# Optimization experiments

Measured on AMD Instinct MI355X. Metric: run time of the kernel, lower is better.

## Reference

```python
import jax, jax.numpy as jnp
import numpy as np

N_E = 1024
E_DIM = 64
BETA = 0.25


def setup_inputs() -> dict:
    key = jax.random.key(0)
    k1, k2 = jax.random.split(key)
    z = jax.random.normal(k1, (32, E_DIM, 32, 32), dtype=jnp.float32)
    embedding = jax.random.uniform(k2, (N_E, E_DIM), dtype=jnp.float32,
                                   minval=-1.0 / N_E, maxval=1.0 / N_E)
    return {"z": z, "embedding": embedding}


def reference(z, embedding):
    beta = BETA
    bt, ch, h, w = z.shape
    n_e = embedding.shape[0]
    # BCHW -> BHWC, flatten to [N, e_dim]
    zp = jnp.transpose(z, (0, 2, 3, 1))
    zf = zp.reshape(-1, ch)
    # squared L2 distances to each codebook entry: [N, n_e]
    d = (jnp.sum(zf ** 2, axis=1, keepdims=True)
         + jnp.sum(embedding ** 2, axis=1)
         - 2.0 * jnp.matmul(zf, embedding.T))
    idx = jnp.argmin(d, axis=1)                      # [N]
    min_encodings = jax.nn.one_hot(idx, n_e, dtype=jnp.float32)  # [N, n_e]
    # gather codebook rows (equivalent to one_hot @ embedding)
    z_q = embedding[idx].reshape(zp.shape)           # [B,H,W,C]
    loss = (jnp.mean((jax.lax.stop_gradient(z_q) - zp) ** 2)
            + beta * jnp.mean((z_q - jax.lax.stop_gradient(zp)) ** 2))
    # straight-through estimator
    z_q_st = zp + jax.lax.stop_gradient(z_q - zp)
    e_mean = jnp.mean(min_encodings, axis=0)
    perplexity = jnp.exp(-jnp.sum(e_mean * jnp.log(e_mean + 1e-10)))
    z_q_out = jnp.transpose(z_q_st, (0, 3, 1, 2))    # back to BCHW
    min_encoding_indices = idx.reshape(bt, h, w)
    return loss, z_q_out, perplexity, min_encodings, min_encoding_indices
```

## Files before the change

kernel.cpp:

```cpp
#include <hip/hip_runtime.h>
#include <cfloat>
#include <cstddef>


#define NROWS 32768
#define NE    1024
#define EDIM  64
#define TPB_A 256
#define GRID_A 2048
#define TPB_B 256
#define GRID_B 512
#define NPART 512

#define OFF_LOSS ((size_t)0)
#define OFF_ZQ   ((size_t)1)
#define OFF_PERP ((size_t)2097153)
#define OFF_OH   ((size_t)2097154)
#define OFF_IDX  ((size_t)35651586)

typedef float v2f __attribute__((ext_vector_type(2)));


__global__ __launch_bounds__(128) void vq_e2(const float* __restrict__ emb,
                                             float* __restrict__ e2buf) {
    int j = blockIdx.x * 128 + threadIdx.x;
    const float* e = emb + ((size_t)j << 6);
    double s = 0.0;
#pragma unroll
    for (int c = 0; c < EDIM; ++c) { float v = e[c]; s += (double)v * (double)v; }
    e2buf[j] = (float)s;
}

__global__ __launch_bounds__(TPB_A, 5) void vq_scan(const float* __restrict__ z,
                                                    const float* __restrict__ emb,
                                                    const float* __restrict__ e2buf,
                                                    float* __restrict__ out) {
    const int t    = threadIdx.x;
    const int lane = t & 63;
    const int q    = t >> 6;
    const int rb   = blockIdx.x >> 2;
    const int cb   = blockIdx.x & 3;
    const int r0   = rb << 6;
    const int qu   = __builtin_amdgcn_readfirstlane(q);

    const int row  = r0 + lane;
    const int b    = row >> 10;
    const int m    = row & 1023;
    const size_t zbase = (size_t)b * 65536 + (size_t)m;

    __shared__ float s_wd[4][64];
    __shared__ int   s_wj[4][64];

    v2f zp[32];
    double sd = 0.0;
#pragma unroll
    for (int n = 0; n < 32; ++n) {
        float x = z[zbase + (size_t)(2 * n) * 1024];
        float y = z[zbase + (size_t)(2 * n + 1) * 1024];
        zp[n] = (v2f){x, y};
        sd += (double)x * (double)x;
        sd += (double)y * (double)y;
    }
    const float z2f = (float)sd;

    float* ohb = out + OFF_OH + (size_t)r0 * 1024 + (cb << 8);

    const int jf = (cb << 8) + (qu << 6);
    float bestd = FLT_MAX;
    int   bestj = 0;
    for (int jj = 0; jj < 64; ++jj) {
        if (!(jj & 1)) {
            int i  = t + (jj >> 1) * TPB_A;
            int r  = i >> 7;
            int c2 = i & 127;
            *(float2*)(ohb + (size_t)r * 1024 + 2 * c2) = make_float2(0.f, 0.f);
        }
        const int j = jf + jj;
        const float4* ep = (const float4*)(emb + ((size_t)j << 6));
        const float e2f = e2buf[j];
        float4 e[16];
#pragma unroll
        for (int k = 0; k < 16; ++k) e[k] = ep[k];
        v2f a01 = {0.f, 0.f}, a23 = {0.f, 0.f};
#pragma unroll
        for (int k = 0; k < 16; ++k) {
            v2f exy = {e[k].x, e[k].y};
            v2f ezw = {e[k].z, e[k].w};
            a01 = __builtin_elementwise_fma(exy, zp[2 * k],     a01);
            a23 = __builtin_elementwise_fma(ezw, zp[2 * k + 1], a23);
        }
        float dot = (a01.x + a01.y) + (a23.x + a23.y);
        float d   = (z2f + e2f) - 2.0f * dot;
        if (d < bestd) { bestd = d; bestj = j; }
    }

    s_wd[q][lane] = bestd;
    s_wj[q][lane] = bestj;
    __syncthreads();
    if (t < 64) {
        float bd = s_wd[0][t];
        int   bj = s_wj[0][t];
#pragma unroll
        for (int w = 1; w < 4; ++w) {
            float dw = s_wd[w][t];
            if (dw < bd) { bd = dw; bj = s_wj[w][t]; }
        }
        const int rr = r0 + t;
        const size_t zb2 = (size_t)(rr >> 10) * 65536 + (size_t)(rr & 1023);
        out[OFF_ZQ + zb2 + (size_t)(2 * cb) * 1024]     = bd;
        out[OFF_ZQ + zb2 + (size_t)(2 * cb + 1) * 1024] = __int_as_float(bj);
    }
}

__global__ __launch_bounds__(TPB_B) void vq_epi(const float* __restrict__ z,
                                                const float* __restrict__ emb,
                                                int* __restrict__ hist,
                                                float* __restrict__ partial,
                                                float* __restrict__ out) {
    const int t    = threadIdx.x;
    const int lane = t & 63;
    const int q    = t >> 6;
    const int r0   = blockIdx.x << 6;

    __shared__ int   s_idx[64];
    __shared__ float s_l[8];

    if (t < 64) {
        const int row = r0 + t;
        const int b   = row >> 10;
        const int m   = row & 1023;
        const size_t zbase = (size_t)b * 65536 + (size_t)m;
        const float* cp = out + OFF_ZQ + zbase;
        float bd = cp[0];
        int   bj = __float_as_int(cp[1024]);
#pragma unroll
        for (int gc = 1; gc < 4; ++gc) {
            float d = cp[(size_t)(2 * gc) * 1024];
            int   j = __float_as_int(cp[(size_t)(2 * gc + 1) * 1024]);
            if (d < bd) { bd = d; bj = j; }
        }
        s_idx[t] = bj;
        out[OFF_IDX + row] = (float)bj;
        out[OFF_OH + (size_t)row * 1024 + bj] = 1.0f;
        atomicAdd(&hist[bj], 1);
    }
    __syncthreads();

    {
        const int row = r0 + lane;
        const int b   = row >> 10;
        const int m   = row & 1023;
        const size_t zbr = (size_t)b * 65536 + (size_t)m;
        const int    jjx = s_idx[lane];
        const float* er  = emb + ((size_t)jjx << 6);
        float* zq = out + OFF_ZQ + zbr;
#pragma unroll
        for (int p = 0; p < 2; ++p) {
            const int cls = q + 4 * p;
            float ls = 0.f;
#pragma unroll
            for (int i = 0; i < 8; ++i) {
                int c = cls + 8 * i;
                float zc   = z[zbr + (size_t)c * 1024];
                float ev   = er[c];
                float diff = ev - zc;
                zq[(size_t)c * 1024] = zc + diff;
                ls = fmaf(diff, diff, ls);
            }
#pragma unroll
            for (int off = 32; off >= 1; off >>= 1) ls += __shfl_down(ls, off);
            if (lane == 0) s_l[cls] = ls;
        }
        __syncthreads();
        if (t == 0) {
            float l = 0.f;
#pragma unroll
            for (int c = 0; c < 8; ++c) l += s_l[c];
            partial[blockIdx.x] = l;
        }
    }
}

__global__ __launch_bounds__(1024) void vq_final(const int* __restrict__ hist,
                                                 const float* __restrict__ partial,
                                                 float* __restrict__ out) {
    int t = threadIdx.x;
    float p    = (float)hist[t] * (1.0f / 32768.0f);
    float term = p * logf(p + 1e-10f);
    float lp   = (t < NPART) ? partial[t] : 0.f;
#pragma unroll
    for (int off = 32; off >= 1; off >>= 1) {
        term += __shfl_down(term, off);
        lp   += __shfl_down(lp, off);
    }
    __shared__ float st[16], sl[16];
    int w = t >> 6, ln = t & 63;
    if (ln == 0) { st[w] = term; sl[w] = lp; }
    __syncthreads();
    if (t == 0) {
        float s = 0.f, l = 0.f;
#pragma unroll
        for (int i = 0; i < 16; ++i) { s += st[i]; l += sl[i]; }
        out[OFF_LOSS] = 1.25f * l * (1.0f / 2097152.0f);
        out[OFF_PERP] = expf(-s);
    }
}

extern "C" void kernel_launch(void* const* d_in, const int* in_sizes, int n_in,
                              void* d_out, int out_size, void* d_ws, size_t ws_size,
                              hipStream_t stream) {
    const float* z   = (const float*)d_in[0];
    const float* emb = (const float*)d_in[1];
    float* out     = (float*)d_out;
    int*   hist    = (int*)d_ws;
    float* partial = (float*)((char*)d_ws + 4096);
    float* e2buf   = (float*)((char*)d_ws + 8192);

    hipMemsetAsync(hist, 0, 4096, stream);
    vq_e2<<<8, 128, 0, stream>>>(emb, e2buf);
    vq_scan<<<GRID_A, TPB_A, 0, stream>>>(z, emb, e2buf, out);
    vq_epi<<<GRID_B, TPB_B, 0, stream>>>(z, emb, hist, partial, out);
    vq_final<<<1, 1024, 0, stream>>>(hist, partial, out);
}
```

Measured before the change: 211.3 us.

## Fuse codebook scan and epilogue into one kernel, fold hist clear into e2

Merges the distance scan and the epilogue into one kernel. Each block now owns 64 rows and all 1024 codes, so the scratch write and re-read of partial argmin results through the z_q buffer goes away. The histogram memset is folded into the e2 kernel, which removes one launch. In exchange the grid shrinks from 2048 to 512 blocks and each wave scans 256 codes serially, which lowers parallelism and occupancy on a large-CU GPU.

```diff
diff --git a/kernel.cpp b/kernel.cpp
--- a/kernel.cpp
+++ b/kernel.cpp
@@ -6,10 +6,8 @@
 #define NROWS 32768
 #define NE    1024
 #define EDIM  64
-#define TPB_A 256
-#define GRID_A 2048
-#define TPB_B 256
-#define GRID_B 512
+#define TPB   256
+#define GRID  512
 #define NPART 512
 
 #define OFF_LOSS ((size_t)0)
@@ -22,8 +20,10 @@
 
 
 __global__ __launch_bounds__(128) void vq_e2(const float* __restrict__ emb,
-                                             float* __restrict__ e2buf) {
+                                             float* __restrict__ e2buf,
+                                             int* __restrict__ hist) {
     int j = blockIdx.x * 128 + threadIdx.x;
+    hist[j] = 0;
     const float* e = emb + ((size_t)j << 6);
     double s = 0.0;
 #pragma unroll
@@ -31,16 +31,16 @@
     e2buf[j] = (float)s;
 }
 
-__global__ __launch_bounds__(TPB_A, 5) void vq_scan(const float* __restrict__ z,
-                                                    const float* __restrict__ emb,
-                                                    const float* __restrict__ e2buf,
-                                                    float* __restrict__ out) {
+__global__ __launch_bounds__(TPB, 5) void vq_fused(const float* __restrict__ z,
+                                                   const float* __restrict__ emb,
+                                                   const float* __restrict__ e2buf,
+                                                   int* __restrict__ hist,
+                                                   float* __restrict__ partial,
+                                                   float* __restrict__ out) {
     const int t    = threadIdx.x;
     const int lane = t & 63;
     const int q    = t >> 6;
-    const int rb   = blockIdx.x >> 2;
-    const int cb   = blockIdx.x & 3;
-    const int r0   = rb << 6;
+    const int r0   = blockIdx.x << 6;
     const int qu   = __builtin_amdgcn_readfirstlane(q);
 
     const int row  = r0 + lane;
@@ -50,6 +50,8 @@
 
     __shared__ float s_wd[4][64];
     __shared__ int   s_wj[4][64];
+    __shared__ int   s_idx[64];
+    __shared__ float s_l[8];
 
     v2f zp[32];
     double sd = 0.0;
@@ -63,16 +65,16 @@
     }
     const float z2f = (float)sd;
 
-    float* ohb = out + OFF_OH + (size_t)r0 * 1024 + (cb << 8);
+    float* ohb = out + OFF_OH + (size_t)r0 * 1024;
 
-    const int jf = (cb << 8) + (qu << 6);
+    const int jf = qu << 8;
     float bestd = FLT_MAX;
     int   bestj = 0;
-    for (int jj = 0; jj < 64; ++jj) {
+    for (int jj = 0; jj < 256; ++jj) {
         if (!(jj & 1)) {
-            int i  = t + (jj >> 1) * TPB_A;
-            int r  = i >> 7;
-            int c2 = i & 127;
+            int i  = t + (jj >> 1) * TPB;
+            int r  = i >> 9;
+            int c2 = i & 511;
             *(float2*)(ohb + (size_t)r * 1024 + 2 * c2) = make_float2(0.f, 0.f);
         }
         const int j = jf + jj;
@@ -105,55 +107,18 @@
             float dw = s_wd[w][t];
             if (dw < bd) { bd = dw; bj = s_wj[w][t]; }
         }
+        s_idx[t] = bj;
         const int rr = r0 + t;
-        const size_t zb2 = (size_t)(rr >> 10) * 65536 + (size_t)(rr & 1023);
-        out[OFF_ZQ + zb2 + (size_t)(2 * cb) * 1024]     = bd;
-        out[OFF_ZQ + zb2 + (size_t)(2 * cb + 1) * 1024] = __int_as_float(bj);
-    }
-}
-
-__global__ __launch_bounds__(TPB_B) void vq_epi(const float* __restrict__ z,
-                                                const float* __restrict__ emb,
-                                                int* __restrict__ hist,
-                                                float* __restrict__ partial,
-                                                float* __restrict__ out) {
-    const int t    = threadIdx.x;
-    const int lane = t & 63;
-    const int q    = t >> 6;
-    const int r0   = blockIdx.x << 6;
-
-    __shared__ int   s_idx[64];
-    __shared__ float s_l[8];
-
-    if (t < 64) {
-        const int row = r0 + t;
-        const int b   = row >> 10;
-        const int m   = row & 1023;
-        const size_t zbase = (size_t)b * 65536 + (size_t)m;
-        const float* cp = out + OFF_ZQ + zbase;
-        float bd = cp[0];
-        int   bj = __float_as_int(cp[1024]);
-#pragma unroll
-        for (int gc = 1; gc < 4; ++gc) {
-            float d = cp[(size_t)(2 * gc) * 1024];
-            int   j = __float_as_int(cp[(size_t)(2 * gc + 1) * 1024]);
-            if (d < bd) { bd = d; bj = j; }
-        }
-        s_idx[t] = bj;
-        out[OFF_IDX + row] = (float)bj;
-        out[OFF_OH + (size_t)row * 1024 + bj] = 1.0f;
+        out[OFF_IDX + rr] = (float)bj;
+        out[OFF_OH + (size_t)rr * 1024 + bj] = 1.0f;
         atomicAdd(&hist[bj], 1);
     }
     __syncthreads();
 
     {
-        const int row = r0 + lane;
-        const int b   = row >> 10;
-        const int m   = row & 1023;
-        const size_t zbr = (size_t)b * 65536 + (size_t)m;
         const int    jjx = s_idx[lane];
         const float* er  = emb + ((size_t)jjx << 6);
-        float* zq = out + OFF_ZQ + zbr;
+        float* zq = out + OFF_ZQ + zbase;
 #pragma unroll
         for (int p = 0; p < 2; ++p) {
             const int cls = q + 4 * p;
@@ -161,7 +126,7 @@
 #pragma unroll
             for (int i = 0; i < 8; ++i) {
                 int c = cls + 8 * i;
-                float zc   = z[zbr + (size_t)c * 1024];
+                float zc   = z[zbase + (size_t)c * 1024];
                 float ev   = er[c];
                 float diff = ev - zc;
                 zq[(size_t)c * 1024] = zc + diff;
@@ -216,9 +181,7 @@
     float* partial = (float*)((char*)d_ws + 4096);
     float* e2buf   = (float*)((char*)d_ws + 8192);
 
-    hipMemsetAsync(hist, 0, 4096, stream);
-    vq_e2<<<8, 128, 0, stream>>>(emb, e2buf);
-    vq_scan<<<GRID_A, TPB_A, 0, stream>>>(z, emb, e2buf, out);
-    vq_epi<<<GRID_B, TPB_B, 0, stream>>>(z, emb, hist, partial, out);
+    vq_e2<<<8, 128, 0, stream>>>(emb, e2buf, hist);
+    vq_fused<<<GRID, TPB, 0, stream>>>(z, emb, e2buf, hist, partial, out);
     vq_final<<<1, 1024, 0, stream>>>(hist, partial, out);
 }
```

Result: slower. 236.4 us (+11.9%).
